# Kernel tuning notes

Measured on AMD Instinct MI355X. Metric: run time of the kernel, lower is better.

## Reference

```python
import jax, jax.numpy as jnp
import numpy as np

RADIUS = 8
EPS = 0.005

_DN = ('NCHW', 'OIHW', 'NCHW')

def _box_filter(t, r):
    """Separable normalized box filter with reflect padding. t: [H, W]."""
    ks = 2 * r + 1
    tp = jnp.pad(t, ((r, r), (r, r)), mode='reflect')[None, None]  # [1,1,H+2r,W+2r]
    kh = jnp.ones((1, 1, 1, ks), t.dtype) / ks
    kv = jnp.ones((1, 1, ks, 1), t.dtype) / ks
    out = jax.lax.conv_general_dilated(tp, kh, (1, 1), 'VALID', dimension_numbers=_DN)
    out = jax.lax.conv_general_dilated(out, kv, (1, 1), 'VALID', dimension_numbers=_DN)
    return out[0, 0]  # [H, W]

def setup_inputs() -> dict:
    key = jax.random.key(0)
    x = jax.random.uniform(key, (4096, 4096, 3), dtype=jnp.float32)
    return {"x": x}

def reference(x):
    # Rec.709 luma
    Y = 0.2126 * x[..., 0] + 0.7152 * x[..., 1] + 0.0722 * x[..., 2]  # [H,W]
    mean_I = _box_filter(Y, RADIUS)
    mean_II = _box_filter(Y * Y, RADIUS)
    var_I = mean_II - mean_I * mean_I
    a = var_I / (var_I + EPS)
    b = mean_I - a * mean_I
    mean_a = _box_filter(a, RADIUS)
    mean_b = _box_filter(b, RADIUS)
    Y_smooth = mean_a * Y + mean_b
    scale = (Y_smooth / jnp.maximum(Y, 1e-6))[..., None]  # [H,W,1]
    return jnp.clip(x * scale, 0.0, 1.0)
```

## Files before the change

kernel.cpp:

```cpp
#include <hip/hip_runtime.h>
#include <hip/hip_fp16.h>


#define HH 4096
#define WW 4096
#define TW 64
#define TH 64
#define SW 96
#define SH 96
#define SYS 98
#define HIS 81
#define HAS 65
#define INV289 (1.0f / 289.0f)
#define EPSV 0.005f

#define R1BYTES 25920
#define R2BYTES 31104

typedef float f32x4 __attribute__((ext_vector_type(4)));

__device__ __forceinline__ int reflect_idx(int i, int n) {
    i = (i < 0) ? -i : i;
    i = (i >= n) ? (2 * n - 2 - i) : i;
    return i;
}

__global__ __launch_bounds__(512, 4) void gf_fused(const float* __restrict__ x,
                                                   float* __restrict__ out) {
    __shared__ __align__(16) char smem[R1BYTES + R2BYTES];
    __half*  sY    = (__half*)smem;
    __half2* ab    = (__half2*)smem;
    __half2* hIhII = (__half2*)(smem + R1BYTES);
    __half2* hAhB  = (__half2*)(smem + R1BYTES);

    const int t = threadIdx.x;
    const int tx = blockIdx.x * TW;
    const int ty = blockIdx.y * TH;

    {
        const bool interior = (tx >= 16) & (tx + SW - 16 <= WW) &
                              (ty >= 16) & (ty + SH - 16 <= HH);
        if (interior) {
            for (int task = t; task < SH * 24; task += 512) {
                int r = task / 24;
                int g = task - r * 24;
                const float4* p = (const float4*)(x + ((long)(ty + r - 16) * WW + (tx - 16 + 4 * g)) * 3);
                float4 f0 = p[0], f1 = p[1], f2 = p[2];
                float Y0 = 0.2126f * f0.x + 0.7152f * f0.y + 0.0722f * f0.z;
                float Y1 = 0.2126f * f0.w + 0.7152f * f1.x + 0.0722f * f1.y;
                float Y2 = 0.2126f * f1.z + 0.7152f * f1.w + 0.0722f * f2.x;
                float Y3 = 0.2126f * f2.y + 0.7152f * f2.z + 0.0722f * f2.w;
                __half2* q2 = (__half2*)&sY[r * SYS + 4 * g];
                q2[0] = __floats2half2_rn(Y0, Y1);
                q2[1] = __floats2half2_rn(Y2, Y3);
            }
        } else {
            for (int task = t; task < SH * 24; task += 512) {
                int r = task / 24;
                int g = task - r * 24;
                int gy = reflect_idx(ty + r - 16, HH);
                #pragma unroll
                for (int cc = 0; cc < 4; ++cc) {
                    int gx = reflect_idx(tx - 16 + 4 * g + cc, WW);
                    const float* p = x + ((long)gy * WW + gx) * 3;
                    float Yv = 0.2126f * p[0] + 0.7152f * p[1] + 0.0722f * p[2];
                    sY[r * SYS + 4 * g + cc] = __float2half_rn(Yv);
                }
            }
        }
    }
    __syncthreads();

    if (t < 480) {
        int r = t % 96;
        int s = t / 96;
        int base = r * SYS + s * 16;
        int ob = r * HIS + s * 16;
        float sI = 0.f, sII = 0.f;
        #pragma unroll
        for (int k = 0; k <= 16; ++k) {
            float w = __half2float(sY[base + k]);
            sI += w; sII += w * w;
        }
        hIhII[ob] = __floats2half2_rn(sI, sII);
        #pragma unroll
        for (int j = 1; j < 16; ++j) {
            float va = __half2float(sY[base + 16 + j]);
            float vs = __half2float(sY[base + j - 1]);
            sI  += va - vs;
            sII += va * va - vs * vs;
            hIhII[ob + j] = __floats2half2_rn(sI, sII);
        }
    }
    __syncthreads();

    if (t < 400) {
        int c = t % 80;
        int q = t / 80;
        int r0 = q * 16;
        float sI = 0.f, sII = 0.f;
        #pragma unroll
        for (int k = 0; k <= 16; ++k) {
            float2 v = __half22float2(hIhII[(r0 + k) * HIS + c]);
            sI += v.x; sII += v.y;
        }
        #pragma unroll
        for (int j = 0; j < 16; ++j) {
            int o = r0 + j;
            float mI = sI * INV289;
            float mII = sII * INV289;
            float var = mII - mI * mI;
            float a = var * __builtin_amdgcn_rcpf(var + EPSV);
            float b = mI - a * mI;
            ab[o * HIS + c] = __floats2half2_rn(a, b);
            if (j < 15) {
                float2 va = __half22float2(hIhII[(o + 17) * HIS + c]);
                float2 vs = __half22float2(hIhII[o * HIS + c]);
                sI  += va.x - vs.x;
                sII += va.y - vs.y;
            }
        }
    }
    __syncthreads();

    if (t < 320) {
        int r = t % 80;
        int s = t / 80;
        int base = r * HIS + s * 16;
        int ob = r * HAS + s * 16;
        float sA = 0.f, sB = 0.f;
        #pragma unroll
        for (int k = 0; k <= 16; ++k) {
            float2 v = __half22float2(ab[base + k]);
            sA += v.x; sB += v.y;
        }
        hAhB[ob] = __floats2half2_rn(sA, sB);
        #pragma unroll
        for (int j = 1; j < 16; ++j) {
            float2 va = __half22float2(ab[base + 16 + j]);
            float2 vs = __half22float2(ab[base + j - 1]);
            sA += va.x - vs.x;
            sB += va.y - vs.y;
            hAhB[ob + j] = __floats2half2_rn(sA, sB);
        }
    }
    __syncthreads();

    {
        const int m  = t & 15;
        const int q  = t >> 4;
        const int r0 = q * 2;
        const int c0 = m * 4;
        float sA[4] = {0.f, 0.f, 0.f, 0.f};
        float sB[4] = {0.f, 0.f, 0.f, 0.f};
        #pragma unroll
        for (int k = 0; k <= 16; ++k) {
            int rb = (r0 + k) * HAS + c0;
            #pragma unroll
            for (int cc = 0; cc < 4; ++cc) {
                float2 v = __half22float2(hAhB[rb + cc]);
                sA[cc] += v.x; sB[cc] += v.y;
            }
        }
        #pragma unroll
        for (int j = 0; j < 2; ++j) {
            int o = r0 + j;
            long gbase = ((long)(ty + o) * WW + (tx + c0)) * 3;
            const float4* p = (const float4*)(x + gbase);
            float4 f0 = p[0], f1 = p[1], f2 = p[2];
            float px[12] = {f0.x, f0.y, f0.z, f0.w, f1.x, f1.y,
                            f1.z, f1.w, f2.x, f2.y, f2.z, f2.w};
            float ov[12];
            #pragma unroll
            for (int cc = 0; cc < 4; ++cc) {
                float rr = px[3 * cc], gg = px[3 * cc + 1], bb = px[3 * cc + 2];
                float Y = 0.2126f * rr + 0.7152f * gg + 0.0722f * bb;
                float ma = sA[cc] * INV289;
                float mb = sB[cc] * INV289;
                float scale = (ma * Y + mb) * __builtin_amdgcn_rcpf(fmaxf(Y, 1e-6f));
                ov[3 * cc]     = fminf(fmaxf(rr * scale, 0.f), 1.f);
                ov[3 * cc + 1] = fminf(fmaxf(gg * scale, 0.f), 1.f);
                ov[3 * cc + 2] = fminf(fmaxf(bb * scale, 0.f), 1.f);
            }
            f32x4* qo = (f32x4*)(out + gbase);
            f32x4 s0 = {ov[0], ov[1], ov[2],  ov[3]};
            f32x4 s1 = {ov[4], ov[5], ov[6],  ov[7]};
            f32x4 s2 = {ov[8], ov[9], ov[10], ov[11]};
            __builtin_nontemporal_store(s0, qo);
            __builtin_nontemporal_store(s1, qo + 1);
            __builtin_nontemporal_store(s2, qo + 2);
            if (j == 0) {
                #pragma unroll
                for (int cc = 0; cc < 4; ++cc) {
                    float2 va = __half22float2(hAhB[(o + 17) * HAS + c0 + cc]);
                    float2 vs = __half22float2(hAhB[o * HAS + c0 + cc]);
                    sA[cc] += va.x - vs.x;
                    sB[cc] += va.y - vs.y;
                }
            }
        }
    }
}

extern "C" void kernel_launch(void* const* d_in, const int* in_sizes, int n_in,
                              void* d_out, int out_size, void* d_ws, size_t ws_size,
                              hipStream_t stream) {
    const float* x = (const float*)d_in[0];
    float* out = (float*)d_out;
    dim3 grid(WW / TW, HH / TH);
    gf_fused<<<grid, 512, 0, stream>>>(x, out);
}
```

Baseline: 358.3 us.

## Vectorize shared-memory access with XOR-swizzled layouts and wider per-thread work

Reworks the shared-memory layout of every filter stage into byte-addressed rows with XOR swizzling, so each stage reads and writes 8- or 16-byte vectors instead of scalar halves. The horizontal passes load a whole row segment into registers first, and the vertical passes handle two columns or four rows per thread. The goal is fewer LDS instructions and fewer bank conflicts. In exchange it uses more registers (32-float arrays), leaves more threads idle in the final stage (256 of 512 active), and adds complex swizzle indexing that could hide correctness bugs.

After: 361.0 us. No clear change (+0.8%).

```diff
diff --git a/kernel.cpp b/kernel.cpp
--- a/kernel.cpp
+++ b/kernel.cpp
@@ -6,16 +6,15 @@
 #define WW 4096
 #define TW 64
 #define TH 64
-#define SW 96
 #define SH 96
-#define SYS 98
-#define HIS 81
-#define HAS 65
+#define SYB 256
+#define HIB 336
+#define ABB 336
+#define HAB 272
+#define R1BYTES 26880
+#define R2BYTES 32256
 #define INV289 (1.0f / 289.0f)
 #define EPSV 0.005f
-
-#define R1BYTES 25920
-#define R2BYTES 31104
 
 typedef float f32x4 __attribute__((ext_vector_type(4)));
 
@@ -25,21 +24,27 @@
     return i;
 }
 
+__device__ __forceinline__ float2 h2f(unsigned u) {
+    union { unsigned u; __half2 h; } c; c.u = u;
+    return __half22float2(c.h);
+}
+__device__ __forceinline__ unsigned f2h(float a, float b) {
+    union { unsigned u; __half2 h; } c; c.h = __floats2half2_rn(a, b);
+    return c.u;
+}
+
 __global__ __launch_bounds__(512, 4) void gf_fused(const float* __restrict__ x,
                                                    float* __restrict__ out) {
     __shared__ __align__(16) char smem[R1BYTES + R2BYTES];
-    __half*  sY    = (__half*)smem;
-    __half2* ab    = (__half2*)smem;
-    __half2* hIhII = (__half2*)(smem + R1BYTES);
-    __half2* hAhB  = (__half2*)(smem + R1BYTES);
+    char* const r2 = smem + R1BYTES;
 
     const int t = threadIdx.x;
     const int tx = blockIdx.x * TW;
     const int ty = blockIdx.y * TH;
 
     {
-        const bool interior = (tx >= 16) & (tx + SW - 16 <= WW) &
-                              (ty >= 16) & (ty + SH - 16 <= HH);
+        const bool interior = (tx >= 16) & (tx + 80 <= WW) &
+                              (ty >= 16) & (ty + 80 <= HH);
         if (interior) {
             for (int task = t; task < SH * 24; task += 512) {
                 int r = task / 24;
@@ -50,9 +55,9 @@
                 float Y1 = 0.2126f * f0.w + 0.7152f * f1.x + 0.0722f * f1.y;
                 float Y2 = 0.2126f * f1.z + 0.7152f * f1.w + 0.0722f * f2.x;
                 float Y3 = 0.2126f * f2.y + 0.7152f * f2.z + 0.0722f * f2.w;
-                __half2* q2 = (__half2*)&sY[r * SYS + 4 * g];
-                q2[0] = __floats2half2_rn(Y0, Y1);
-                q2[1] = __floats2half2_rn(Y2, Y3);
+                int wb = r * SYB + ((((g >> 1) ^ (r & 7)) << 4) | ((g & 1) << 3));
+                uint2 wv; wv.x = f2h(Y0, Y1); wv.y = f2h(Y2, Y3);
+                *(uint2*)(smem + wb) = wv;
             }
         } else {
             for (int task = t; task < SH * 24; task += 512) {
@@ -64,7 +69,9 @@
                     int gx = reflect_idx(tx - 16 + 4 * g + cc, WW);
                     const float* p = x + ((long)gy * WW + gx) * 3;
                     float Yv = 0.2126f * p[0] + 0.7152f * p[1] + 0.0722f * p[2];
-                    sY[r * SYS + 4 * g + cc] = __float2half_rn(Yv);
+                    int cb = 8 * g + 2 * cc;
+                    int wb = r * SYB + ((((cb >> 4) ^ (r & 7)) << 4) | (cb & 15));
+                    *(__half*)(smem + wb) = __float2half_rn(Yv);
                 }
             }
         }
@@ -72,98 +79,121 @@
     __syncthreads();
 
     if (t < 480) {
-        int r = t % 96;
-        int s = t / 96;
-        int base = r * SYS + s * 16;
-        int ob = r * HIS + s * 16;
+        int s = t % 5, r = t / 5;
+        int u = r & 7;
+        float w[32];
+        #pragma unroll
+        for (int k = 0; k < 4; ++k) {
+            uint4 v = *(const uint4*)(smem + r * SYB + (((2 * s + k) ^ u) << 4));
+            float2 f;
+            f = h2f(v.x); w[8 * k + 0] = f.x; w[8 * k + 1] = f.y;
+            f = h2f(v.y); w[8 * k + 2] = f.x; w[8 * k + 3] = f.y;
+            f = h2f(v.z); w[8 * k + 4] = f.x; w[8 * k + 5] = f.y;
+            f = h2f(v.w); w[8 * k + 6] = f.x; w[8 * k + 7] = f.y;
+        }
         float sI = 0.f, sII = 0.f;
         #pragma unroll
+        for (int k = 0; k <= 16; ++k) { sI += w[k]; sII += w[k] * w[k]; }
+        unsigned o32[4];
+        #pragma unroll
+        for (int j = 0; j < 16; ++j) {
+            if (j > 0) {
+                float va = w[16 + j], vs = w[j - 1];
+                sI += va - vs; sII += va * va - vs * vs;
+            }
+            o32[j & 3] = f2h(sI, sII);
+            if ((j & 3) == 3) {
+                uint4 q; q.x = o32[0]; q.y = o32[1]; q.z = o32[2]; q.w = o32[3];
+                *(uint4*)(r2 + r * HIB + s * 64 + (j >> 2) * 16) = q;
+            }
+        }
+    }
+    __syncthreads();
+
+    if (t < 400) {
+        int cp = t % 40, q = t / 40;
+        int r0 = q * 8;
+        float sI0 = 0.f, sII0 = 0.f, sI1 = 0.f, sII1 = 0.f;
+        #pragma unroll
         for (int k = 0; k <= 16; ++k) {
-            float w = __half2float(sY[base + k]);
-            sI += w; sII += w * w;
-        }
-        hIhII[ob] = __floats2half2_rn(sI, sII);
-        #pragma unroll
-        for (int j = 1; j < 16; ++j) {
-            float va = __half2float(sY[base + 16 + j]);
-            float vs = __half2float(sY[base + j - 1]);
-            sI  += va - vs;
-            sII += va * va - vs * vs;
-            hIhII[ob + j] = __floats2half2_rn(sI, sII);
-        }
-    }
-    __syncthreads();
-
-    if (t < 400) {
-        int c = t % 80;
-        int q = t / 80;
-        int r0 = q * 16;
-        float sI = 0.f, sII = 0.f;
-        #pragma unroll
-        for (int k = 0; k <= 16; ++k) {
-            float2 v = __half22float2(hIhII[(r0 + k) * HIS + c]);
-            sI += v.x; sII += v.y;
-        }
+            uint2 v = *(const uint2*)(r2 + (r0 + k) * HIB + cp * 8);
+            float2 f0 = h2f(v.x), f1 = h2f(v.y);
+            sI0 += f0.x; sII0 += f0.y; sI1 += f1.x; sII1 += f1.y;
+        }
+        #pragma unroll
+        for (int j = 0; j < 8; ++j) {
+            int o = r0 + j;
+            float mI0 = sI0 * INV289, mII0 = sII0 * INV289;
+            float var0 = mII0 - mI0 * mI0;
+            float a0 = var0 * __builtin_amdgcn_rcpf(var0 + EPSV);
+            float b0 = mI0 - a0 * mI0;
+            float mI1 = sI1 * INV289, mII1 = sII1 * INV289;
+            float var1 = mII1 - mI1 * mI1;
+            float a1 = var1 * __builtin_amdgcn_rcpf(var1 + EPSV);
+            float b1 = mI1 - a1 * mI1;
+            uint2 wv; wv.x = f2h(a0, b0); wv.y = f2h(a1, b1);
+            *(uint2*)(smem + o * ABB + cp * 8) = wv;
+            if (j < 7) {
+                uint2 va = *(const uint2*)(r2 + (o + 17) * HIB + cp * 8);
+                uint2 vs = *(const uint2*)(r2 + o * HIB + cp * 8);
+                float2 fa0 = h2f(va.x), fa1 = h2f(va.y);
+                float2 fs0 = h2f(vs.x), fs1 = h2f(vs.y);
+                sI0 += fa0.x - fs0.x; sII0 += fa0.y - fs0.y;
+                sI1 += fa1.x - fs1.x; sII1 += fa1.y - fs1.y;
+            }
+        }
+    }
+    __syncthreads();
+
+    if (t < 320) {
+        int s = t % 4, r = t / 4;
+        float av[32], bv[32];
+        #pragma unroll
+        for (int k = 0; k < 8; ++k) {
+            uint4 v = *(const uint4*)(smem + r * ABB + s * 64 + k * 16);
+            float2 f;
+            f = h2f(v.x); av[4 * k + 0] = f.x; bv[4 * k + 0] = f.y;
+            f = h2f(v.y); av[4 * k + 1] = f.x; bv[4 * k + 1] = f.y;
+            f = h2f(v.z); av[4 * k + 2] = f.x; bv[4 * k + 2] = f.y;
+            f = h2f(v.w); av[4 * k + 3] = f.x; bv[4 * k + 3] = f.y;
+        }
+        float sA = 0.f, sB = 0.f;
+        #pragma unroll
+        for (int k = 0; k <= 16; ++k) { sA += av[k]; sB += bv[k]; }
+        int u = r & 7;
+        unsigned o32[4];
         #pragma unroll
         for (int j = 0; j < 16; ++j) {
-            int o = r0 + j;
-            float mI = sI * INV289;
-            float mII = sII * INV289;
-            float var = mII - mI * mI;
-            float a = var * __builtin_amdgcn_rcpf(var + EPSV);
-            float b = mI - a * mI;
-            ab[o * HIS + c] = __floats2half2_rn(a, b);
-            if (j < 15) {
-                float2 va = __half22float2(hIhII[(o + 17) * HIS + c]);
-                float2 vs = __half22float2(hIhII[o * HIS + c]);
-                sI  += va.x - vs.x;
-                sII += va.y - vs.y;
-            }
-        }
-    }
-    __syncthreads();
-
-    if (t < 320) {
-        int r = t % 80;
-        int s = t / 80;
-        int base = r * HIS + s * 16;
-        int ob = r * HAS + s * 16;
-        float sA = 0.f, sB = 0.f;
-        #pragma unroll
-        for (int k = 0; k <= 16; ++k) {
-            float2 v = __half22float2(ab[base + k]);
-            sA += v.x; sB += v.y;
-        }
-        hAhB[ob] = __floats2half2_rn(sA, sB);
-        #pragma unroll
-        for (int j = 1; j < 16; ++j) {
-            float2 va = __half22float2(ab[base + 16 + j]);
-            float2 vs = __half22float2(ab[base + j - 1]);
-            sA += va.x - vs.x;
-            sB += va.y - vs.y;
-            hAhB[ob + j] = __floats2half2_rn(sA, sB);
-        }
-    }
-    __syncthreads();
-
-    {
-        const int m  = t & 15;
-        const int q  = t >> 4;
-        const int r0 = q * 2;
-        const int c0 = m * 4;
+            if (j > 0) {
+                sA += av[16 + j] - av[j - 1];
+                sB += bv[16 + j] - bv[j - 1];
+            }
+            o32[j & 3] = f2h(sA, sB);
+            if ((j & 3) == 3) {
+                uint4 q; q.x = o32[0]; q.y = o32[1]; q.z = o32[2]; q.w = o32[3];
+                *(uint4*)(r2 + r * HAB + (((4 * s + (j >> 2)) ^ u) << 4)) = q;
+            }
+        }
+    }
+    __syncthreads();
+
+    if (t < 256) {
+        int m = t & 15, rg = t >> 4;
+        int c0 = 4 * m, r0 = 4 * rg;
         float sA[4] = {0.f, 0.f, 0.f, 0.f};
         float sB[4] = {0.f, 0.f, 0.f, 0.f};
         #pragma unroll
         for (int k = 0; k <= 16; ++k) {
-            int rb = (r0 + k) * HAS + c0;
-            #pragma unroll
-            for (int cc = 0; cc < 4; ++cc) {
-                float2 v = __half22float2(hAhB[rb + cc]);
-                sA[cc] += v.x; sB[cc] += v.y;
-            }
-        }
-        #pragma unroll
-        for (int j = 0; j < 2; ++j) {
+            int rr = r0 + k;
+            uint4 v = *(const uint4*)(r2 + rr * HAB + ((m ^ (rr & 7)) << 4));
+            float2 f;
+            f = h2f(v.x); sA[0] += f.x; sB[0] += f.y;
+            f = h2f(v.y); sA[1] += f.x; sB[1] += f.y;
+            f = h2f(v.z); sA[2] += f.x; sB[2] += f.y;
+            f = h2f(v.w); sA[3] += f.x; sB[3] += f.y;
+        }
+        #pragma unroll
+        for (int j = 0; j < 4; ++j) {
             int o = r0 + j;
             long gbase = ((long)(ty + o) * WW + (tx + c0)) * 3;
             const float4* p = (const float4*)(x + gbase);
@@ -189,14 +219,15 @@
             __builtin_nontemporal_store(s0, qo);
             __builtin_nontemporal_store(s1, qo + 1);
             __builtin_nontemporal_store(s2, qo + 2);
-            if (j == 0) {
-                #pragma unroll
-                for (int cc = 0; cc < 4; ++cc) {
-                    float2 va = __half22float2(hAhB[(o + 17) * HAS + c0 + cc]);
-                    float2 vs = __half22float2(hAhB[o * HAS + c0 + cc]);
-                    sA[cc] += va.x - vs.x;
-                    sB[cc] += va.y - vs.y;
-                }
+            if (j < 3) {
+                int ra = o + 17, rs = o;
+                uint4 va = *(const uint4*)(r2 + ra * HAB + ((m ^ (ra & 7)) << 4));
+                uint4 vs = *(const uint4*)(r2 + rs * HAB + ((m ^ (rs & 7)) << 4));
+                float2 fa, fs;
+                fa = h2f(va.x); fs = h2f(vs.x); sA[0] += fa.x - fs.x; sB[0] += fa.y - fs.y;
+                fa = h2f(va.y); fs = h2f(vs.y); sA[1] += fa.x - fs.x; sB[1] += fa.y - fs.y;
+                fa = h2f(va.z); fs = h2f(vs.z); sA[2] += fa.x - fs.x; sB[2] += fa.y - fs.y;
+                fa = h2f(va.w); fs = h2f(vs.w); sA[3] += fa.x - fs.x; sB[3] += fa.y - fs.y;
             }
         }
     }
```

## Shrink tile height to 32 rows and vectorize final vertical box pass

Applied to the files above, without the earlier changes.

Halves the output tile height from 64 to 32 rows. That cuts shared memory per block so more blocks can be resident, and the launch bound now asks for 8 blocks instead of 4. The horizontal a/b pass now writes 16-byte packed vectors into a padded layout, and the final pass reads them with uint4 loads, one output row per thread. The cost is more halo overhead: each 32-row tile still loads and filters a 64-row input window, so redundant luma loads and box sums grow relative to output.

Result: no change. 359.1 us (+0.2%).

```diff
diff --git a/kernel.cpp b/kernel.cpp
--- a/kernel.cpp
+++ b/kernel.cpp
@@ -1,21 +1,19 @@
 #include <hip/hip_runtime.h>
 #include <hip/hip_fp16.h>
-
 
 #define HH 4096
 #define WW 4096
 #define TW 64
-#define TH 64
-#define SW 96
-#define SH 96
+#define TH 32
+#define SH 64
 #define SYS 98
 #define HIS 81
-#define HAS 65
+#define ABS 81
+#define HAS 68
+#define R1BYTES 15552
+#define R2BYTES 20736
 #define INV289 (1.0f / 289.0f)
 #define EPSV 0.005f
-
-#define R1BYTES 25920
-#define R2BYTES 31104
 
 typedef float f32x4 __attribute__((ext_vector_type(4)));
 
@@ -25,21 +23,21 @@
     return i;
 }
 
-__global__ __launch_bounds__(512, 4) void gf_fused(const float* __restrict__ x,
+__global__ __launch_bounds__(512, 8) void gf_fused(const float* __restrict__ x,
                                                    float* __restrict__ out) {
     __shared__ __align__(16) char smem[R1BYTES + R2BYTES];
+    char* const r2m = smem + R1BYTES;
     __half*  sY    = (__half*)smem;
     __half2* ab    = (__half2*)smem;
-    __half2* hIhII = (__half2*)(smem + R1BYTES);
-    __half2* hAhB  = (__half2*)(smem + R1BYTES);
+    __half2* hIhII = (__half2*)r2m;
 
     const int t = threadIdx.x;
     const int tx = blockIdx.x * TW;
     const int ty = blockIdx.y * TH;
 
     {
-        const bool interior = (tx >= 16) & (tx + SW - 16 <= WW) &
-                              (ty >= 16) & (ty + SH - 16 <= HH);
+        const bool interior = (tx >= 16) & (tx + 80 <= WW) &
+                              (ty >= 16) & (ty + 48 <= HH);
         if (interior) {
             for (int task = t; task < SH * 24; task += 512) {
                 int r = task / 24;
@@ -71,9 +69,9 @@
     }
     __syncthreads();
 
-    if (t < 480) {
-        int r = t % 96;
-        int s = t / 96;
+    if (t < 320) {
+        int r = t & 63;
+        int s = t >> 6;
         int base = r * SYS + s * 16;
         int ob = r * HIS + s * 16;
         float sI = 0.f, sII = 0.f;
@@ -94,10 +92,10 @@
     }
     __syncthreads();
 
-    if (t < 400) {
+    if (t < 480) {
         int c = t % 80;
         int q = t / 80;
-        int r0 = q * 16;
+        int r0 = q * 8;
         float sI = 0.f, sII = 0.f;
         #pragma unroll
         for (int k = 0; k <= 16; ++k) {
@@ -105,15 +103,15 @@
             sI += v.x; sII += v.y;
         }
         #pragma unroll
-        for (int j = 0; j < 16; ++j) {
+        for (int j = 0; j < 8; ++j) {
             int o = r0 + j;
             float mI = sI * INV289;
             float mII = sII * INV289;
             float var = mII - mI * mI;
             float a = var * __builtin_amdgcn_rcpf(var + EPSV);
             float b = mI - a * mI;
-            ab[o * HIS + c] = __floats2half2_rn(a, b);
-            if (j < 15) {
+            ab[o * ABS + c] = __floats2half2_rn(a, b);
+            if (j < 7) {
                 float2 va = __half22float2(hIhII[(o + 17) * HIS + c]);
                 float2 vs = __half22float2(hIhII[o * HIS + c]);
                 sI  += va.x - vs.x;
@@ -123,82 +121,77 @@
     }
     __syncthreads();
 
-    if (t < 320) {
-        int r = t % 80;
-        int s = t / 80;
-        int base = r * HIS + s * 16;
-        int ob = r * HAS + s * 16;
+    if (t < 384) {
+        int s = t & 7;
+        int r = t >> 3;
+        int base = r * ABS + s * 8;
         float sA = 0.f, sB = 0.f;
         #pragma unroll
         for (int k = 0; k <= 16; ++k) {
             float2 v = __half22float2(ab[base + k]);
             sA += v.x; sB += v.y;
         }
-        hAhB[ob] = __floats2half2_rn(sA, sB);
-        #pragma unroll
-        for (int j = 1; j < 16; ++j) {
-            float2 va = __half22float2(ab[base + 16 + j]);
-            float2 vs = __half22float2(ab[base + j - 1]);
-            sA += va.x - vs.x;
-            sB += va.y - vs.y;
-            hAhB[ob + j] = __floats2half2_rn(sA, sB);
+        unsigned o32[4];
+        #pragma unroll
+        for (int j = 0; j < 8; ++j) {
+            if (j > 0) {
+                float2 va = __half22float2(ab[base + 16 + j]);
+                float2 vs = __half22float2(ab[base + j - 1]);
+                sA += va.x - vs.x;
+                sB += va.y - vs.y;
+            }
+            union { unsigned u; __half2 h; } cv;
+            cv.h = __floats2half2_rn(sA, sB);
+            o32[j & 3] = cv.u;
+            if ((j & 3) == 3) {
+                uint4 qv; qv.x = o32[0]; qv.y = o32[1]; qv.z = o32[2]; qv.w = o32[3];
+                *(uint4*)(r2m + r * 272 + s * 32 + (j >> 2) * 16) = qv;
+            }
         }
     }
     __syncthreads();
 
     {
-        const int m  = t & 15;
-        const int q  = t >> 4;
-        const int r0 = q * 2;
-        const int c0 = m * 4;
-        float sA[4] = {0.f, 0.f, 0.f, 0.f};
-        float sB[4] = {0.f, 0.f, 0.f, 0.f};
-        #pragma unroll
-        for (int k = 0; k <= 16; ++k) {
-            int rb = (r0 + k) * HAS + c0;
-            #pragma unroll
-            for (int cc = 0; cc < 4; ++cc) {
-                float2 v = __half22float2(hAhB[rb + cc]);
-                sA[cc] += v.x; sB[cc] += v.y;
-            }
-        }
-        #pragma unroll
-        for (int j = 0; j < 2; ++j) {
-            int o = r0 + j;
-            long gbase = ((long)(ty + o) * WW + (tx + c0)) * 3;
-            const float4* p = (const float4*)(x + gbase);
-            float4 f0 = p[0], f1 = p[1], f2 = p[2];
-            float px[12] = {f0.x, f0.y, f0.z, f0.w, f1.x, f1.y,
-                            f1.z, f1.w, f2.x, f2.y, f2.z, f2.w};
-            float ov[12];
-            #pragma unroll
-            for (int cc = 0; cc < 4; ++cc) {
-                float rr = px[3 * cc], gg = px[3 * cc + 1], bb = px[3 * cc + 2];
-                float Y = 0.2126f * rr + 0.7152f * gg + 0.0722f * bb;
-                float ma = sA[cc] * INV289;
-                float mb = sB[cc] * INV289;
-                float scale = (ma * Y + mb) * __builtin_amdgcn_rcpf(fmaxf(Y, 1e-6f));
-                ov[3 * cc]     = fminf(fmaxf(rr * scale, 0.f), 1.f);
-                ov[3 * cc + 1] = fminf(fmaxf(gg * scale, 0.f), 1.f);
-                ov[3 * cc + 2] = fminf(fmaxf(bb * scale, 0.f), 1.f);
-            }
-            f32x4* qo = (f32x4*)(out + gbase);
-            f32x4 s0 = {ov[0], ov[1], ov[2],  ov[3]};
-            f32x4 s1 = {ov[4], ov[5], ov[6],  ov[7]};
-            f32x4 s2 = {ov[8], ov[9], ov[10], ov[11]};
-            __builtin_nontemporal_store(s0, qo);
-            __builtin_nontemporal_store(s1, qo + 1);
-            __builtin_nontemporal_store(s2, qo + 2);
-            if (j == 0) {
-                #pragma unroll
-                for (int cc = 0; cc < 4; ++cc) {
-                    float2 va = __half22float2(hAhB[(o + 17) * HAS + c0 + cc]);
-                    float2 vs = __half22float2(hAhB[o * HAS + c0 + cc]);
-                    sA[cc] += va.x - vs.x;
-                    sB[cc] += va.y - vs.y;
-                }
-            }
-        }
+        const int m = t & 15;
+        const int r = t >> 4;
+        float sA0 = 0.f, sA1 = 0.f, sA2 = 0.f, sA3 = 0.f;
+        float sB0 = 0.f, sB1 = 0.f, sB2 = 0.f, sB3 = 0.f;
+        #pragma unroll
+        for (int k = 0; k <= 16; ++k) {
+            uint4 v = *(const uint4*)(r2m + (r + k) * 272 + m * 16);
+            union { unsigned u; __half2 h; } c0, c1, c2, c3;
+            c0.u = v.x; c1.u = v.y; c2.u = v.z; c3.u = v.w;
+            float2 f0 = __half22float2(c0.h), f1 = __half22float2(c1.h);
+            float2 f2 = __half22float2(c2.h), f3 = __half22float2(c3.h);
+            sA0 += f0.x; sB0 += f0.y;
+            sA1 += f1.x; sB1 += f1.y;
+            sA2 += f2.x; sB2 += f2.y;
+            sA3 += f3.x; sB3 += f3.y;
+        }
+        float maf[4] = {sA0 * INV289, sA1 * INV289, sA2 * INV289, sA3 * INV289};
+        float mbf[4] = {sB0 * INV289, sB1 * INV289, sB2 * INV289, sB3 * INV289};
+        long gbase = ((long)(ty + r) * WW + (tx + 4 * m)) * 3;
+        const float4* p = (const float4*)(x + gbase);
+        float4 f0 = p[0], f1 = p[1], f2 = p[2];
+        float px[12] = {f0.x, f0.y, f0.z, f0.w, f1.x, f1.y,
+                        f1.z, f1.w, f2.x, f2.y, f2.z, f2.w};
+        float ov[12];
+        #pragma unroll
+        for (int cc = 0; cc < 4; ++cc) {
+            float rr = px[3 * cc], gg = px[3 * cc + 1], bb = px[3 * cc + 2];
+            float Y = 0.2126f * rr + 0.7152f * gg + 0.0722f * bb;
+            float scale = (maf[cc] * Y + mbf[cc]) * __builtin_amdgcn_rcpf(fmaxf(Y, 1e-6f));
+            ov[3 * cc]     = fminf(fmaxf(rr * scale, 0.f), 1.f);
+            ov[3 * cc + 1] = fminf(fmaxf(gg * scale, 0.f), 1.f);
+            ov[3 * cc + 2] = fminf(fmaxf(bb * scale, 0.f), 1.f);
+        }
+        f32x4* qo = (f32x4*)(out + gbase);
+        f32x4 s0 = {ov[0], ov[1], ov[2],  ov[3]};
+        f32x4 s1 = {ov[4], ov[5], ov[6],  ov[7]};
+        f32x4 s2 = {ov[8], ov[9], ov[10], ov[11]};
+        __builtin_nontemporal_store(s0, qo);
+        __builtin_nontemporal_store(s1, qo + 1);
+        __builtin_nontemporal_store(s2, qo + 2);
     }
 }
 
```
